# Kernel optimization log

Measured on AMD Instinct MI355X. Metric: run time of the kernel, lower is better.

## Reference

```python
import jax, jax.numpy as jnp
import numpy as np

N_NODES = 50000
N_EDGES = 800000
IN_FEAT = 256
OUT_FEAT = 256
NUM_RELS = 8
NUM_BASES = 4


def setup_inputs() -> dict:
    key = jax.random.key(0)
    ks = jax.random.split(key, 8)
    feat = jax.random.normal(ks[0], (N_NODES, IN_FEAT), dtype=jnp.float32)
    norm = jax.random.uniform(ks[1], (N_EDGES, 1), dtype=jnp.float32)
    src = jax.random.randint(ks[2], (N_EDGES,), 0, N_NODES)
    dst = jax.random.randint(ks[3], (N_EDGES,), 0, N_NODES)
    etypes = jax.random.randint(ks[4], (N_EDGES,), 0, NUM_RELS)
    # learned parameters (xavier-ish scale)
    weight = jax.random.normal(ks[5], (NUM_BASES, IN_FEAT, OUT_FEAT), dtype=jnp.float32) * (2.0 / np.sqrt(IN_FEAT + OUT_FEAT))
    w_comp = jax.random.normal(ks[6], (NUM_RELS, NUM_BASES), dtype=jnp.float32) * (2.0 / np.sqrt(NUM_RELS + NUM_BASES))
    loop_weight = jax.random.normal(ks[7], (IN_FEAT, OUT_FEAT), dtype=jnp.float32) * (2.0 / np.sqrt(IN_FEAT + OUT_FEAT))
    h_bias = jnp.zeros((OUT_FEAT,), dtype=jnp.float32)
    return {"feat": feat, "weight": weight, "w_comp": w_comp,
            "loop_weight": loop_weight, "h_bias": h_bias,
            "norm": norm, "src": src, "dst": dst, "etypes": etypes}


def reference(feat, weight, w_comp, loop_weight, h_bias, norm, src, dst, etypes):
    # basis decomposition: W_r = sum_b a_{rb} V_b  -> [R, in, out]
    W = jnp.einsum('rb,bio->rio', w_comp, weight)
    # relation-grouped GEMM: transform every node by every relation. [N, R, out]
    Hr = jnp.einsum('ni,rio->nro', feat, W)
    # per-edge message: gather (src node, edge relation) then apply edge norm. [E, out]
    msg = Hr[src, etypes] * norm
    # scatter-reduce (sum) messages to destination nodes. [N, out]
    agg = jax.ops.segment_sum(msg, dst, num_segments=N_NODES)
    # self-loop + bias + activation (dropout rate 0.0 -> identity)
    out = agg + feat @ loop_weight + h_bias
    return jax.nn.relu(out)
```

## Files before the change

kernel.cpp:

```cpp
#include <hip/hip_runtime.h>
#include <stdint.h>

typedef unsigned short u16;
typedef __bf16 bf16x8 __attribute__((ext_vector_type(8)));
typedef float f32x4 __attribute__((ext_vector_type(4)));

#define N_NODES 50000
#define N_PAD   50048
#define NUM_E   800000
#define FDIM    256
#define NREL    8
#define NBASE   4
#define KBLK    5
#define NKSTEP  20
#define NSEG    N_NODES
#define NBLK    49
#define MTILES  196

#define PREP_FEAT_BLOCKS 12512
#define PREP_WT_BLOCKS   1280
#define PREP_ZERO_BLOCKS 196

__device__ __forceinline__ u16 f2bf(float f) {
  uint32_t u = __float_as_uint(f);
  u += 0x7FFFu + ((u >> 16) & 1u);
  return (u16)(u >> 16);
}
__device__ __forceinline__ float bf2f(u16 h) {
  return __uint_as_float(((uint32_t)h) << 16);
}

__device__ __forceinline__ void gload_lds16(const void* g, void* l) {
  __builtin_amdgcn_global_load_lds(
      (__attribute__((address_space(1))) uint32_t*)(void*)(uintptr_t)g,
      (__attribute__((address_space(3))) uint32_t*)(uintptr_t)l,
      16, 0, 0);
}

__global__ __launch_bounds__(256) void prep_k(const float* __restrict__ feat,
                                              const float* __restrict__ weight,
                                              const float* __restrict__ loop_w,
                                              u16* __restrict__ fb,
                                              u16* __restrict__ Wb_all,
                                              int* __restrict__ cnt) {
  const int b = blockIdx.x;
  const int tid = threadIdx.x;
  if (b < PREP_FEAT_BLOCKS) {
    int idx = b * 256 + tid;
    int row = idx >> 6;
    int q = (idx & 63) * 4;
    float4 v = make_float4(0.f, 0.f, 0.f, 0.f);
    if (row < N_NODES) v = *reinterpret_cast<const float4*>(feat + (size_t)row * FDIM + q);
    ushort4 h;
    h.x = f2bf(v.x); h.y = f2bf(v.y); h.z = f2bf(v.z); h.w = f2bf(v.w);
    *reinterpret_cast<ushort4*>(fb + (size_t)row * FDIM + q) = h;
  } else if (b < PREP_FEAT_BLOCKS + PREP_WT_BLOCKS) {
    int idx = (b - PREP_FEAT_BLOCKS) * 256 + tid;
    int r = idx >> 16, rem = idx & 65535;
    int o = rem >> 8, i = rem & 255;
    float s = (r < NBASE) ? weight[(size_t)r * 65536 + i * 256 + o]
                          : loop_w[i * 256 + o];
    Wb_all[idx] = f2bf(s);
  } else {
    int i = (b - PREP_FEAT_BLOCKS - PREP_WT_BLOCKS) * 256 + tid;
    if (i < NSEG) cnt[i] = 0;
  }
}

__global__ __launch_bounds__(256) void hist_k(const int* __restrict__ dst,
                                              int* __restrict__ cnt) {
  int e = blockIdx.x * 256 + threadIdx.x;
  if (e < NUM_E) atomicAdd(&cnt[dst[e]], 1);
}

__global__ __launch_bounds__(1024) void scan1(const int* __restrict__ cnt,
                                              int* __restrict__ rowstart,
                                              int* __restrict__ blocksum) {
  __shared__ int wtot[16], woff[16];
  const int tid = threadIdx.x, lane = tid & 63, w = tid >> 6;
  const int i = blockIdx.x * 1024 + tid;
  const int v = (i < NSEG) ? cnt[i] : 0;
  int inc = v;
#pragma unroll
  for (int off = 1; off < 64; off <<= 1) {
    int t = __shfl_up(inc, off);
    if (lane >= off) inc += t;
  }
  if (lane == 63) wtot[w] = inc;
  __syncthreads();
  if (w == 0) {
    int tv = (lane < 16) ? wtot[lane] : 0;
    int tinc = tv;
#pragma unroll
    for (int off = 1; off < 16; off <<= 1) {
      int t = __shfl_up(tinc, off);
      if (lane >= off) tinc += t;
    }
    if (lane < 16) woff[lane] = tinc - tv;
    if (lane == 15) blocksum[blockIdx.x] = tinc;
  }
  __syncthreads();
  if (i < NSEG) rowstart[i] = inc - v + woff[w];
}

__global__ __launch_bounds__(512) void scan2(int* __restrict__ blocksum) {
  __shared__ int s[512];
  const int tid = threadIdx.x;
  const int v = (tid < NBLK) ? blocksum[tid] : 0;
  s[tid] = v;
#pragma unroll
  for (int off = 1; off < 512; off <<= 1) {
    __syncthreads();
    int t = (tid >= off) ? s[tid - off] : 0;
    __syncthreads();
    s[tid] += t;
  }
  if (tid < NBLK) blocksum[tid] = s[tid] - v;
}

__global__ __launch_bounds__(1024) void scan3(int* __restrict__ rowstart,
                                              const int* __restrict__ blockoff,
                                              int* __restrict__ cursor) {
  const int i = blockIdx.x * 1024 + threadIdx.x;
  if (i < NSEG) {
    const int v = rowstart[i] + blockoff[i >> 10];
    rowstart[i] = v;
    cursor[i] = v;
  }
  if (i == NSEG) rowstart[NSEG] = NUM_E;
}

__global__ __launch_bounds__(256) void bucket_k(const int* __restrict__ src,
                                                const int* __restrict__ dst,
                                                const int* __restrict__ et,
                                                const float* __restrict__ norm,
                                                int* __restrict__ cursor,
                                                int* __restrict__ keys,
                                                float* __restrict__ norms) {
  int e = blockIdx.x * 256 + threadIdx.x;
  if (e >= NUM_E) return;
  const int pos = atomicAdd(&cursor[dst[e]], 1);
  keys[pos]  = src[e] * NREL + et[e];
  norms[pos] = norm[e];
}

__global__ __launch_bounds__(256) void agg_G(const u16* __restrict__ feat_bf,
                                             const int* __restrict__ rowstart,
                                             const int* __restrict__ keys,
                                             const float* __restrict__ norms,
                                             const float* __restrict__ w_comp,
                                             u16* __restrict__ G) {
  __shared__ float wcs[NREL * NBASE];
  if (threadIdx.x < NREL * NBASE) wcs[threadIdx.x] = w_comp[threadIdx.x];
  __syncthreads();
  const int n = blockIdx.x * 4 + (threadIdx.x >> 6);
  const int lane = threadIdx.x & 63;
  const int beg = rowstart[n], end = rowstart[n + 1];

  f32x4 acc[NBASE] = {};
  for (int base = beg; base < end; base += 64) {
    const int m = min(64, end - base);
    int kv = 0; float nv = 0.f;
    if (lane < m) { kv = keys[base + lane]; nv = norms[base + lane]; }
    int key = __shfl(kv, 0);
    float nm = __shfl(nv, 0);
    ushort4 h = *reinterpret_cast<const ushort4*>(
        feat_bf + (size_t)(key >> 3) * FDIM + lane * 4);
    for (int j = 0; j < m; ++j) {
      ushort4 h2; int key2 = 0; float nm2 = 0.f;
      if (j + 1 < m) {
        key2 = __shfl(kv, j + 1);
        nm2 = __shfl(nv, j + 1);
        h2 = *reinterpret_cast<const ushort4*>(
            feat_bf + (size_t)(key2 >> 3) * FDIM + lane * 4);
      }
      const int et = key & 7;
      const float f0 = bf2f(h.x), f1 = bf2f(h.y), f2 = bf2f(h.z), f3 = bf2f(h.w);
#pragma unroll
      for (int bb = 0; bb < NBASE; ++bb) {
        const float c = nm * wcs[et * NBASE + bb];
        acc[bb][0] += f0 * c;
        acc[bb][1] += f1 * c;
        acc[bb][2] += f2 * c;
        acc[bb][3] += f3 * c;
      }
      h = h2; key = key2; nm = nm2;
    }
  }
#pragma unroll
  for (int bb = 0; bb < NBASE; ++bb) {
    ushort4 hh;
    hh.x = f2bf(acc[bb][0]);
    hh.y = f2bf(acc[bb][1]);
    hh.z = f2bf(acc[bb][2]);
    hh.w = f2bf(acc[bb][3]);
    *reinterpret_cast<ushort4*>(G + (size_t)n * (NBASE * FDIM) + bb * FDIM + lane * 4) = hh;
  }
}

__global__ __launch_bounds__(512, 2) void fused_gemm(const u16* __restrict__ G,
                                                     const u16* __restrict__ feat_bf,
                                                     const u16* __restrict__ Wb_all,
                                                     const float* __restrict__ bias,
                                                     float* __restrict__ out) {
  __shared__ __align__(16) u16 As[2][256 * 64];
  __shared__ __align__(16) u16 Bs[2][256 * 64];
  const int tid = threadIdx.x;
  const int lane = tid & 63;
  const int w = tid >> 6;
  const int wm = w >> 2, wn = w & 3;
  const int mtile = blockIdx.x;

  const int srow = tid >> 3;
  const int scolx = ((tid & 7) << 3) ^ ((srow & 7) << 3);

  f32x4 acc[8][4] = {};

  auto stage = [&](int ks, int buf) {
    const int r = ks >> 2, kk4 = ks & 3;
    const int kcol = kk4 * 64 + scolx;
#pragma unroll
    for (int q = 0; q < 4; ++q) {
      const int arow = q * 64 + srow;
      int gr = mtile * 256 + arow;
      if (gr >= N_PAD) gr = N_PAD - 1;
      const u16* asrc = (r < NBASE)
          ? G + (size_t)gr * 1024 + r * 256 + kcol
          : feat_bf + (size_t)gr * 256 + kcol;
      gload_lds16(asrc, &As[buf][q * 4096 + tid * 8]);
      const u16* bsrc = Wb_all + (size_t)r * 65536 + (size_t)arow * 256 + kcol;
      gload_lds16(bsrc, &Bs[buf][q * 4096 + tid * 8]);
    }
  };

  stage(0, 0);
  __syncthreads();
  for (int t = 0; t < NKSTEP; ++t) {
    const int cur = t & 1;
    if (t + 1 < NKSTEP) stage(t + 1, cur ^ 1);
#pragma unroll
    for (int kk = 0; kk < 2; ++kk) {
      const int colx = (kk * 32 + ((lane >> 4) << 3)) ^ ((lane & 7) << 3);
      bf16x8 a[8], b[4];
#pragma unroll
      for (int mf = 0; mf < 8; ++mf)
        a[mf] = *reinterpret_cast<const bf16x8*>(
            &As[cur][(wm * 128 + mf * 16 + (lane & 15)) * 64 + colx]);
#pragma unroll
      for (int nf = 0; nf < 4; ++nf)
        b[nf] = *reinterpret_cast<const bf16x8*>(
            &Bs[cur][(wn * 64 + nf * 16 + (lane & 15)) * 64 + colx]);
      __builtin_amdgcn_s_setprio(1);
#pragma unroll
      for (int mf = 0; mf < 8; ++mf)
#pragma unroll
        for (int nf = 0; nf < 4; ++nf)
          acc[mf][nf] = __builtin_amdgcn_mfma_f32_16x16x32_bf16(b[nf], a[mf], acc[mf][nf], 0, 0, 0);
      __builtin_amdgcn_s_setprio(0);
    }
    __syncthreads();
  }

#pragma unroll
  for (int mf = 0; mf < 8; ++mf) {
    const int m = mtile * 256 + wm * 128 + mf * 16 + (lane & 15);
    if (m >= N_NODES) continue;
#pragma unroll
    for (int nf = 0; nf < 4; ++nf) {
      const int o0 = wn * 64 + nf * 16 + ((lane >> 4) << 2);
      const float4 bv = *reinterpret_cast<const float4*>(bias + o0);
      float4 v;
      v.x = fmaxf(acc[mf][nf][0] + bv.x, 0.f);
      v.y = fmaxf(acc[mf][nf][1] + bv.y, 0.f);
      v.z = fmaxf(acc[mf][nf][2] + bv.z, 0.f);
      v.w = fmaxf(acc[mf][nf][3] + bv.w, 0.f);
      *reinterpret_cast<float4*>(out + (size_t)m * 256 + o0) = v;
    }
  }
}

extern "C" void kernel_launch(void* const* d_in, const int* in_sizes, int n_in,
                              void* d_out, int out_size, void* d_ws, size_t ws_size,
                              hipStream_t stream) {
  (void)in_sizes; (void)n_in; (void)out_size; (void)ws_size;
  const float* feat   = (const float*)d_in[0];
  const float* weight = (const float*)d_in[1];
  const float* w_comp = (const float*)d_in[2];
  const float* loop_w = (const float*)d_in[3];
  const float* h_bias = (const float*)d_in[4];
  const float* norm   = (const float*)d_in[5];
  const int*   src    = (const int*)d_in[6];
  const int*   dst    = (const int*)d_in[7];
  const int*   et     = (const int*)d_in[8];
  float* out = (float*)d_out;

  char* ws = (char*)d_ws;
  u16*   feat_bf  = (u16*)(ws);
  u16*   Wb_all   = (u16*)(ws + 25624576);
  u16*   G        = (u16*)(ws + 26279936);
  int*   counts   = (int*)(ws + 128778240);
  int*   rowstart = (int*)(ws + 128978432);
  int*   cursor   = (int*)(ws + 129178880);
  int*   keys     = (int*)(ws + 129379072);
  float* norms    = (float*)(ws + 132579072);
  int*   blocksum = (int*)(ws + 135779072);

  prep_k<<<PREP_FEAT_BLOCKS + PREP_WT_BLOCKS + PREP_ZERO_BLOCKS, 256, 0, stream>>>(
      feat, weight, loop_w, feat_bf, Wb_all, counts);

  hist_k<<<(NUM_E + 255) / 256, 256, 0, stream>>>(dst, counts);
  scan1<<<NBLK, 1024, 0, stream>>>(counts, rowstart, blocksum);
  scan2<<<1, 512, 0, stream>>>(blocksum);
  scan3<<<NBLK + 1, 1024, 0, stream>>>(rowstart, blocksum, cursor);
  bucket_k<<<(NUM_E + 255) / 256, 256, 0, stream>>>(src, dst, et, norm, cursor, keys, norms);

  agg_G<<<N_NODES / 4, 256, 0, stream>>>(feat_bf, rowstart, keys, norms, w_comp, G);

  fused_gemm<<<MTILES, 512, 0, stream>>>(G, feat_bf, Wb_all, h_bias, out);
}
```

Baseline: 229.1 us.

## Accumulate per relation, batch eight gathers, and pack edge key and norm

```diff
diff --git a/kernel.cpp b/kernel.cpp
--- a/kernel.cpp
+++ b/kernel.cpp
@@ -135,67 +135,93 @@
                                                 const int* __restrict__ et,
                                                 const float* __restrict__ norm,
                                                 int* __restrict__ cursor,
-                                                int* __restrict__ keys,
-                                                float* __restrict__ norms) {
+                                                int2* __restrict__ ekv) {
   int e = blockIdx.x * 256 + threadIdx.x;
   if (e >= NUM_E) return;
   const int pos = atomicAdd(&cursor[dst[e]], 1);
-  keys[pos]  = src[e] * NREL + et[e];
-  norms[pos] = norm[e];
+  int2 kv;
+  kv.x = src[e] * NREL + et[e];
+  kv.y = __float_as_int(norm[e]);
+  ekv[pos] = kv;
 }
 
 __global__ __launch_bounds__(256) void agg_G(const u16* __restrict__ feat_bf,
                                              const int* __restrict__ rowstart,
-                                             const int* __restrict__ keys,
-                                             const float* __restrict__ norms,
+                                             const int2* __restrict__ ekv,
                                              const float* __restrict__ w_comp,
                                              u16* __restrict__ G) {
-  __shared__ float wcs[NREL * NBASE];
-  if (threadIdx.x < NREL * NBASE) wcs[threadIdx.x] = w_comp[threadIdx.x];
+  __shared__ float4 wcs4[NREL];
+  if (threadIdx.x < NREL) {
+    const float* wr = w_comp + threadIdx.x * NBASE;
+    wcs4[threadIdx.x] = make_float4(wr[0], wr[1], wr[2], wr[3]);
+  }
   __syncthreads();
   const int n = blockIdx.x * 4 + (threadIdx.x >> 6);
   const int lane = threadIdx.x & 63;
   const int beg = rowstart[n], end = rowstart[n + 1];
 
-  f32x4 acc[NBASE] = {};
+  f32x4 a0 = {}, a1 = {}, a2 = {}, a3 = {}, a4 = {}, a5 = {}, a6 = {}, a7 = {};
+  const u16* fl = feat_bf + lane * 4;
+
   for (int base = beg; base < end; base += 64) {
     const int m = min(64, end - base);
-    int kv = 0; float nv = 0.f;
-    if (lane < m) { kv = keys[base + lane]; nv = norms[base + lane]; }
-    int key = __shfl(kv, 0);
-    float nm = __shfl(nv, 0);
-    ushort4 h = *reinterpret_cast<const ushort4*>(
-        feat_bf + (size_t)(key >> 3) * FDIM + lane * 4);
-    for (int j = 0; j < m; ++j) {
-      ushort4 h2; int key2 = 0; float nm2 = 0.f;
-      if (j + 1 < m) {
-        key2 = __shfl(kv, j + 1);
-        nm2 = __shfl(nv, j + 1);
-        h2 = *reinterpret_cast<const ushort4*>(
-            feat_bf + (size_t)(key2 >> 3) * FDIM + lane * 4);
+    int kvi = 0, nvi = 0;
+    if (lane < m) {
+      const int2 e = ekv[base + lane];
+      kvi = e.x; nvi = e.y;
+    }
+#pragma unroll
+    for (int g = 0; g < 8; ++g) {
+      if (g * 8 >= m) break;
+      ushort4 h[8];
+      int ks[8]; float ns[8];
+#pragma unroll
+      for (int jj = 0; jj < 8; ++jj) {
+        const int j = g * 8 + jj;
+        ks[jj] = __builtin_amdgcn_readlane(kvi, j);
+        ns[jj] = __uint_as_float((unsigned)__builtin_amdgcn_readlane(nvi, j));
+        h[jj] = *reinterpret_cast<const ushort4*>(
+            fl + ((size_t)((unsigned)ks[jj] >> 3) << 8));
       }
-      const int et = key & 7;
-      const float f0 = bf2f(h.x), f1 = bf2f(h.y), f2 = bf2f(h.z), f3 = bf2f(h.w);
-#pragma unroll
-      for (int bb = 0; bb < NBASE; ++bb) {
-        const float c = nm * wcs[et * NBASE + bb];
-        acc[bb][0] += f0 * c;
-        acc[bb][1] += f1 * c;
-        acc[bb][2] += f2 * c;
-        acc[bb][3] += f3 * c;
+#pragma unroll
+      for (int jj = 0; jj < 8; ++jj) {
+        const float nm = ns[jj];
+        const float f0 = bf2f(h[jj].x), f1 = bf2f(h[jj].y),
+                    f2 = bf2f(h[jj].z), f3 = bf2f(h[jj].w);
+        switch (ks[jj] & 7) {
+          case 0: a0[0]+=f0*nm; a0[1]+=f1*nm; a0[2]+=f2*nm; a0[3]+=f3*nm; break;
+          case 1: a1[0]+=f0*nm; a1[1]+=f1*nm; a1[2]+=f2*nm; a1[3]+=f3*nm; break;
+          case 2: a2[0]+=f0*nm; a2[1]+=f1*nm; a2[2]+=f2*nm; a2[3]+=f3*nm; break;
+          case 3: a3[0]+=f0*nm; a3[1]+=f1*nm; a3[2]+=f2*nm; a3[3]+=f3*nm; break;
+          case 4: a4[0]+=f0*nm; a4[1]+=f1*nm; a4[2]+=f2*nm; a4[3]+=f3*nm; break;
+          case 5: a5[0]+=f0*nm; a5[1]+=f1*nm; a5[2]+=f2*nm; a5[3]+=f3*nm; break;
+          case 6: a6[0]+=f0*nm; a6[1]+=f1*nm; a6[2]+=f2*nm; a6[3]+=f3*nm; break;
+          default: a7[0]+=f0*nm; a7[1]+=f1*nm; a7[2]+=f2*nm; a7[3]+=f3*nm; break;
+        }
       }
-      h = h2; key = key2; nm = nm2;
-    }
-  }
-#pragma unroll
-  for (int bb = 0; bb < NBASE; ++bb) {
-    ushort4 hh;
-    hh.x = f2bf(acc[bb][0]);
-    hh.y = f2bf(acc[bb][1]);
-    hh.z = f2bf(acc[bb][2]);
-    hh.w = f2bf(acc[bb][3]);
-    *reinterpret_cast<ushort4*>(G + (size_t)n * (NBASE * FDIM) + bb * FDIM + lane * 4) = hh;
-  }
+    }
+  }
+
+  f32x4 c0 = {}, c1 = {}, c2 = {}, c3 = {};
+#define COMB(AR, R) { const float4 w = wcs4[R];                          \
+    c0[0]+=w.x*AR[0]; c0[1]+=w.x*AR[1]; c0[2]+=w.x*AR[2]; c0[3]+=w.x*AR[3]; \
+    c1[0]+=w.y*AR[0]; c1[1]+=w.y*AR[1]; c1[2]+=w.y*AR[2]; c1[3]+=w.y*AR[3]; \
+    c2[0]+=w.z*AR[0]; c2[1]+=w.z*AR[1]; c2[2]+=w.z*AR[2]; c2[3]+=w.z*AR[3]; \
+    c3[0]+=w.w*AR[0]; c3[1]+=w.w*AR[1]; c3[2]+=w.w*AR[2]; c3[3]+=w.w*AR[3]; }
+  COMB(a0, 0) COMB(a1, 1) COMB(a2, 2) COMB(a3, 3)
+  COMB(a4, 4) COMB(a5, 5) COMB(a6, 6) COMB(a7, 7)
+#undef COMB
+
+  const size_t gbase = (size_t)n * (NBASE * FDIM) + lane * 4;
+  ushort4 hh;
+  hh.x = f2bf(c0[0]); hh.y = f2bf(c0[1]); hh.z = f2bf(c0[2]); hh.w = f2bf(c0[3]);
+  *reinterpret_cast<ushort4*>(G + gbase + 0 * FDIM) = hh;
+  hh.x = f2bf(c1[0]); hh.y = f2bf(c1[1]); hh.z = f2bf(c1[2]); hh.w = f2bf(c1[3]);
+  *reinterpret_cast<ushort4*>(G + gbase + 1 * FDIM) = hh;
+  hh.x = f2bf(c2[0]); hh.y = f2bf(c2[1]); hh.z = f2bf(c2[2]); hh.w = f2bf(c2[3]);
+  *reinterpret_cast<ushort4*>(G + gbase + 2 * FDIM) = hh;
+  hh.x = f2bf(c3[0]); hh.y = f2bf(c3[1]); hh.z = f2bf(c3[2]); hh.w = f2bf(c3[3]);
+  *reinterpret_cast<ushort4*>(G + gbase + 3 * FDIM) = hh;
 }
 
 __global__ __launch_bounds__(512, 2) void fused_gemm(const u16* __restrict__ G,
@@ -301,8 +327,7 @@
   int*   counts   = (int*)(ws + 128778240);
   int*   rowstart = (int*)(ws + 128978432);
   int*   cursor   = (int*)(ws + 129178880);
-  int*   keys     = (int*)(ws + 129379072);
-  float* norms    = (float*)(ws + 132579072);
+  int2*  ekv      = (int2*)(ws + 129379072);
   int*   blocksum = (int*)(ws + 135779072);
 
   prep_k<<<PREP_FEAT_BLOCKS + PREP_WT_BLOCKS + PREP_ZERO_BLOCKS, 256, 0, stream>>>(
@@ -312,9 +337,9 @@
   scan1<<<NBLK, 1024, 0, stream>>>(counts, rowstart, blocksum);
   scan2<<<1, 512, 0, stream>>>(blocksum);
   scan3<<<NBLK + 1, 1024, 0, stream>>>(rowstart, blocksum, cursor);
-  bucket_k<<<(NUM_E + 255) / 256, 256, 0, stream>>>(src, dst, et, norm, cursor, keys, norms);
-
-  agg_G<<<N_NODES / 4, 256, 0, stream>>>(feat_bf, rowstart, keys, norms, w_comp, G);
+  bucket_k<<<(NUM_E + 255) / 256, 256, 0, stream>>>(src, dst, et, norm, cursor, ekv);
+
+  agg_G<<<N_NODES / 4, 256, 0, stream>>>(feat_bf, rowstart, ekv, w_comp, G);
 
   fused_gemm<<<MTILES, 512, 0, stream>>>(G, feat_bf, Wb_all, h_bias, out);
 }
```

Result: no change. 229.9 us (+0.3%).

## Fuse CSR build into one persistent kernel with grid barriers; pack key/norm

Applied to the files above, without the earlier changes.

```diff
diff --git a/kernel.cpp b/kernel.cpp
--- a/kernel.cpp
+++ b/kernel.cpp
@@ -11,15 +11,13 @@
 #define FDIM    256
 #define NREL    8
 #define NBASE   4
-#define KBLK    5
 #define NKSTEP  20
 #define NSEG    N_NODES
-#define NBLK    49
 #define MTILES  196
+#define CSRB    49
 
 #define PREP_FEAT_BLOCKS 12512
 #define PREP_WT_BLOCKS   1280
-#define PREP_ZERO_BLOCKS 196
 
 __device__ __forceinline__ u16 f2bf(float f) {
   uint32_t u = __float_as_uint(f);
@@ -41,8 +39,7 @@
                                               const float* __restrict__ weight,
                                               const float* __restrict__ loop_w,
                                               u16* __restrict__ fb,
-                                              u16* __restrict__ Wb_all,
-                                              int* __restrict__ cnt) {
+                                              u16* __restrict__ Wb_all) {
   const int b = blockIdx.x;
   const int tid = threadIdx.x;
   if (b < PREP_FEAT_BLOCKS) {
@@ -54,32 +51,52 @@
     ushort4 h;
     h.x = f2bf(v.x); h.y = f2bf(v.y); h.z = f2bf(v.z); h.w = f2bf(v.w);
     *reinterpret_cast<ushort4*>(fb + (size_t)row * FDIM + q) = h;
-  } else if (b < PREP_FEAT_BLOCKS + PREP_WT_BLOCKS) {
+  } else {
     int idx = (b - PREP_FEAT_BLOCKS) * 256 + tid;
     int r = idx >> 16, rem = idx & 65535;
     int o = rem >> 8, i = rem & 255;
     float s = (r < NBASE) ? weight[(size_t)r * 65536 + i * 256 + o]
                           : loop_w[i * 256 + o];
     Wb_all[idx] = f2bf(s);
-  } else {
-    int i = (b - PREP_FEAT_BLOCKS - PREP_WT_BLOCKS) * 256 + tid;
-    if (i < NSEG) cnt[i] = 0;
-  }
-}
-
-__global__ __launch_bounds__(256) void hist_k(const int* __restrict__ dst,
-                                              int* __restrict__ cnt) {
-  int e = blockIdx.x * 256 + threadIdx.x;
-  if (e < NUM_E) atomicAdd(&cnt[dst[e]], 1);
-}
-
-__global__ __launch_bounds__(1024) void scan1(const int* __restrict__ cnt,
+  }
+}
+
+__global__ __launch_bounds__(1024) void csr_k(const int* __restrict__ src,
+                                              const int* __restrict__ dst,
+                                              const int* __restrict__ et,
+                                              const float* __restrict__ norm,
+                                              int* __restrict__ cnt,
+                                              int* __restrict__ bar,
                                               int* __restrict__ rowstart,
+                                              int* __restrict__ cursor,
+                                              int2* __restrict__ ekv,
                                               int* __restrict__ blocksum) {
-  __shared__ int wtot[16], woff[16];
-  const int tid = threadIdx.x, lane = tid & 63, w = tid >> 6;
-  const int i = blockIdx.x * 1024 + tid;
-  const int v = (i < NSEG) ? cnt[i] : 0;
+  __shared__ int wtot[16], woff[16], sboff[64];
+  const int tid = threadIdx.x, bid = blockIdx.x;
+  const int lane = tid & 63, w = tid >> 6;
+  const int gtid = bid * 1024 + tid;
+  const int gthreads = CSRB * 1024;
+
+  auto gbar = [&](int target) {
+    __threadfence();
+    __syncthreads();
+    if (tid == 0) {
+      atomicAdd(bar, 1);
+      while (atomicAdd(bar, 0) < target) __builtin_amdgcn_s_sleep(2);
+    }
+    __syncthreads();
+    __threadfence();
+  };
+
+  for (int e = gtid; e < NUM_E; e += gthreads)
+    atomicAdd(&cnt[dst[e]], 1);
+
+  gbar(CSRB);
+
+  const int i = gtid;
+  const int v = (i < NSEG)
+      ? __hip_atomic_load(&cnt[i], __ATOMIC_RELAXED, __HIP_MEMORY_SCOPE_AGENT)
+      : 0;
   int inc = v;
 #pragma unroll
   for (int off = 1; off < 64; off <<= 1) {
@@ -97,57 +114,49 @@
       if (lane >= off) tinc += t;
     }
     if (lane < 16) woff[lane] = tinc - tv;
-    if (lane == 15) blocksum[blockIdx.x] = tinc;
-  }
-  __syncthreads();
-  if (i < NSEG) rowstart[i] = inc - v + woff[w];
-}
-
-__global__ __launch_bounds__(512) void scan2(int* __restrict__ blocksum) {
-  __shared__ int s[512];
-  const int tid = threadIdx.x;
-  const int v = (tid < NBLK) ? blocksum[tid] : 0;
-  s[tid] = v;
-#pragma unroll
-  for (int off = 1; off < 512; off <<= 1) {
-    __syncthreads();
-    int t = (tid >= off) ? s[tid - off] : 0;
-    __syncthreads();
-    s[tid] += t;
-  }
-  if (tid < NBLK) blocksum[tid] = s[tid] - v;
-}
-
-__global__ __launch_bounds__(1024) void scan3(int* __restrict__ rowstart,
-                                              const int* __restrict__ blockoff,
-                                              int* __restrict__ cursor) {
-  const int i = blockIdx.x * 1024 + threadIdx.x;
+    if (lane == 15)
+      __hip_atomic_store(&blocksum[bid], tinc, __ATOMIC_RELAXED, __HIP_MEMORY_SCOPE_AGENT);
+  }
+  __syncthreads();
+  const int local_ex = inc - v + woff[w];
+
+  gbar(2 * CSRB);
+
+  if (tid < 64) {
+    int bv = (tid < CSRB)
+        ? __hip_atomic_load(&blocksum[tid], __ATOMIC_RELAXED, __HIP_MEMORY_SCOPE_AGENT)
+        : 0;
+    int binc = bv;
+#pragma unroll
+    for (int off = 1; off < 64; off <<= 1) {
+      int t = __shfl_up(binc, off);
+      if (tid >= off) binc += t;
+    }
+    sboff[tid] = binc - bv;
+  }
+  __syncthreads();
+  const int boff = sboff[bid];
   if (i < NSEG) {
-    const int v = rowstart[i] + blockoff[i >> 10];
-    rowstart[i] = v;
-    cursor[i] = v;
+    const int rv = local_ex + boff;
+    rowstart[i] = rv;
+    __hip_atomic_store(&cursor[i], rv, __ATOMIC_RELAXED, __HIP_MEMORY_SCOPE_AGENT);
   }
   if (i == NSEG) rowstart[NSEG] = NUM_E;
-}
-
-__global__ __launch_bounds__(256) void bucket_k(const int* __restrict__ src,
-                                                const int* __restrict__ dst,
-                                                const int* __restrict__ et,
-                                                const float* __restrict__ norm,
-                                                int* __restrict__ cursor,
-                                                int* __restrict__ keys,
-                                                float* __restrict__ norms) {
-  int e = blockIdx.x * 256 + threadIdx.x;
-  if (e >= NUM_E) return;
-  const int pos = atomicAdd(&cursor[dst[e]], 1);
-  keys[pos]  = src[e] * NREL + et[e];
-  norms[pos] = norm[e];
+
+  gbar(3 * CSRB);
+
+  for (int e = gtid; e < NUM_E; e += gthreads) {
+    const int pos = atomicAdd(&cursor[dst[e]], 1);
+    int2 kv;
+    kv.x = src[e] * NREL + et[e];
+    kv.y = __float_as_int(norm[e]);
+    ekv[pos] = kv;
+  }
 }
 
 __global__ __launch_bounds__(256) void agg_G(const u16* __restrict__ feat_bf,
                                              const int* __restrict__ rowstart,
-                                             const int* __restrict__ keys,
-                                             const float* __restrict__ norms,
+                                             const int2* __restrict__ ekv,
                                              const float* __restrict__ w_comp,
                                              u16* __restrict__ G) {
   __shared__ float wcs[NREL * NBASE];
@@ -161,7 +170,10 @@
   for (int base = beg; base < end; base += 64) {
     const int m = min(64, end - base);
     int kv = 0; float nv = 0.f;
-    if (lane < m) { kv = keys[base + lane]; nv = norms[base + lane]; }
+    if (lane < m) {
+      const int2 e = ekv[base + lane];
+      kv = e.x; nv = __int_as_float(e.y);
+    }
     int key = __shfl(kv, 0);
     float nm = __shfl(nv, 0);
     ushort4 h = *reinterpret_cast<const ushort4*>(
@@ -299,22 +311,21 @@
   u16*   Wb_all   = (u16*)(ws + 25624576);
   u16*   G        = (u16*)(ws + 26279936);
   int*   counts   = (int*)(ws + 128778240);
+  int*   bar      = (int*)(ws + 128978240);
   int*   rowstart = (int*)(ws + 128978432);
   int*   cursor   = (int*)(ws + 129178880);
-  int*   keys     = (int*)(ws + 129379072);
-  float* norms    = (float*)(ws + 132579072);
+  int2*  ekv      = (int2*)(ws + 129379072);
   int*   blocksum = (int*)(ws + 135779072);
 
-  prep_k<<<PREP_FEAT_BLOCKS + PREP_WT_BLOCKS + PREP_ZERO_BLOCKS, 256, 0, stream>>>(
-      feat, weight, loop_w, feat_bf, Wb_all, counts);
-
-  hist_k<<<(NUM_E + 255) / 256, 256, 0, stream>>>(dst, counts);
-  scan1<<<NBLK, 1024, 0, stream>>>(counts, rowstart, blocksum);
-  scan2<<<1, 512, 0, stream>>>(blocksum);
-  scan3<<<NBLK + 1, 1024, 0, stream>>>(rowstart, blocksum, cursor);
-  bucket_k<<<(NUM_E + 255) / 256, 256, 0, stream>>>(src, dst, et, norm, cursor, keys, norms);
-
-  agg_G<<<N_NODES / 4, 256, 0, stream>>>(feat_bf, rowstart, keys, norms, w_comp, G);
+  hipMemsetAsync(counts, 0, NSEG * sizeof(int) + 192, stream);
+
+  prep_k<<<PREP_FEAT_BLOCKS + PREP_WT_BLOCKS, 256, 0, stream>>>(
+      feat, weight, loop_w, feat_bf, Wb_all);
+
+  csr_k<<<CSRB, 1024, 0, stream>>>(src, dst, et, norm, counts, bar,
+                                   rowstart, cursor, ekv, blocksum);
+
+  agg_G<<<N_NODES / 4, 256, 0, stream>>>(feat_bf, rowstart, ekv, w_comp, G);
 
   fused_gemm<<<MTILES, 512, 0, stream>>>(G, feat_bf, Wb_all, h_bias, out);
 }
```

Result: slower. 327.8 us (+43.1%).
